# Optimization experiments

Measured on AMD Instinct MI355X. Metric: run time of the kernel, lower is better.

Reference implementation:

```python
import jax, jax.numpy as jnp
import numpy as np

D_MODEL = 1024
H = 16
T = 1024
B = 8

def setup_inputs() -> dict:
    key = jax.random.key(0)
    k0, k1, k2, k3, k4 = jax.random.split(key, 5)
    return {
        "x": jax.random.normal(k0, (B, T, D_MODEL), dtype=jnp.float32),
        "Wq": jax.random.normal(k1, (D_MODEL, D_MODEL), dtype=jnp.float32),
        "Wk": jax.random.normal(k2, (D_MODEL, D_MODEL), dtype=jnp.float32),
        "Wv": jax.random.normal(k3, (D_MODEL, D_MODEL), dtype=jnp.float32),
        "Wp": jax.random.normal(k4, (D_MODEL, D_MODEL), dtype=jnp.float32),
    }

def reference(x, Wq, Wk, Wv, Wp):
    b, t, d = x.shape
    dh = d // H
    # projections
    q = (x @ Wq).reshape(b, t, H, dh)
    k = (x @ Wk).reshape(b, t, H, dh)
    v = (x @ Wv).reshape(b, t, H, dh)
    # [b, h, t, t] attention scores, scaled by sqrt(d_head)
    scores = jnp.einsum("bqhd,bkhd->bhqk", q, k) / jnp.sqrt(jnp.float32(dh))
    attn = jax.nn.softmax(scores, axis=-1)
    # [b, h, t, dh] -> [b, t, d]
    out = jnp.einsum("bhqk,bkhd->bqhd", attn, v).reshape(b, t, d)
    return out @ Wp
```

## Files before the change

### kernel.cpp

```cpp
#include <hip/hip_runtime.h>
#include <math.h>


typedef unsigned short u16;
typedef unsigned int u32;
typedef __bf16  bf16x8 __attribute__((ext_vector_type(8)));
typedef unsigned short u16x8 __attribute__((ext_vector_type(8)));
typedef unsigned short u16x4 __attribute__((ext_vector_type(4)));
typedef short s16x4 __attribute__((ext_vector_type(4)));
typedef unsigned int u32x2 __attribute__((ext_vector_type(2)));
typedef float f32x4 __attribute__((ext_vector_type(4)));

#define MFMA16(a,b,c) __builtin_amdgcn_mfma_f32_16x16x32_bf16((a),(b),(c),0,0,0)
#define MFMA16K16(a,b,c) __builtin_amdgcn_mfma_f32_16x16x16bf16_1k((a),(b),(c),0,0,0)

static __device__ __forceinline__ u16 f2b(float f){
  unsigned u = __builtin_bit_cast(unsigned, f);
  u += 0x7fffu + ((u >> 16) & 1u);
  return (u16)(u >> 16);
}
static __device__ __forceinline__ float b2f(u16 h){
  unsigned u = ((unsigned)h) << 16;
  return __builtin_bit_cast(float, u);
}
static __device__ __forceinline__ bf16x8 ldsfrag(const u16* p){
  return __builtin_bit_cast(bf16x8, *(const u16x8*)p);
}
static __device__ __forceinline__ u32 packhi(float fa, float fb){
  return __builtin_amdgcn_perm(__builtin_bit_cast(u32, fa),
                               __builtin_bit_cast(u32, fb), 0x07060302u);
}
static __device__ __forceinline__ void gld16(const void* g, void* l){
  __builtin_amdgcn_global_load_lds(
      (const __attribute__((address_space(1))) void*)g,
      (__attribute__((address_space(3))) void*)l, 16, 0, 0);
}


__global__ __launch_bounds__(256) void split_x_kernel(
    const float* __restrict__ x, u16* __restrict__ xh, u16* __restrict__ xl, int n)
{
  int i = (blockIdx.x * 256 + threadIdx.x) * 8;
  if (i >= n) return;
  float4 v0 = *(const float4*)(x + i);
  float4 v1 = *(const float4*)(x + i + 4);
  float vv[8] = {v0.x, v0.y, v0.z, v0.w, v1.x, v1.y, v1.z, v1.w};
  u16x8 hv, lv;
#pragma unroll
  for (int j = 0; j < 8; j++){
    u16 hb = f2b(vv[j]);
    hv[j] = hb;
    lv[j] = f2b(vv[j] - b2f(hb));
  }
  *(u16x8*)(xh + i) = hv;
  *(u16x8*)(xl + i) = lv;
}

__global__ __launch_bounds__(256) void transpose_split_kernel(
    const float* __restrict__ W, u16* __restrict__ Th, u16* __restrict__ Tl,
    int KD, int ND)
{
  __shared__ float t[32][33];
  int n0 = blockIdx.x * 32, k0 = blockIdx.y * 32;
  int tx = threadIdx.x, ty = threadIdx.y;
#pragma unroll
  for (int i = 0; i < 4; i++){
    int k = k0 + ty + i * 8;
    t[ty + i * 8][tx] = W[(size_t)k * ND + n0 + tx];
  }
  __syncthreads();
#pragma unroll
  for (int i = 0; i < 4; i++){
    int n = n0 + ty + i * 8;
    float v = t[tx][ty + i * 8];
    u16 h = f2b(v);
    Th[(size_t)n * KD + k0 + tx] = h;
    if (Tl) Tl[(size_t)n * KD + k0 + tx] = f2b(v - b2f(h));
  }
}

__global__ __launch_bounds__(256) void vfrag_kernel(
    const u16* __restrict__ V, u16* __restrict__ Vf)
{
  int d = threadIdx.x;
  int tt = (blockIdx.x * 4 + threadIdx.y) * 4;
  int bh = blockIdx.y;
  int b = bh >> 4, h = bh & 15;
  u16x4 vals;
#pragma unroll
  for (int j = 0; j < 4; j++)
    vals[j] = V[(size_t)(b * 1024 + tt + j) * 1024 + h * 64 + d];
  int ktile = tt >> 7, fkt = (tt >> 4) & 7, q = (tt >> 2) & 3;
  int nd = d >> 4, l15 = d & 15;
  size_t idx = ((((size_t)(bh * 8 + ktile) * 8 + fkt) * 4 + nd) * 64 + q * 16 + l15) * 4;
  *(u16x4*)(Vf + idx) = vals;
}

template<int OUTBF16>
__global__ __launch_bounds__(256) void gemm_bt_kernel(
    const u16* __restrict__ A, const u16* __restrict__ Bt, void* __restrict__ Cv,
    int M, int N, int K)
{
  __shared__ __attribute__((aligned(16))) u16 lA[4096], lB[4096];
  const int tid = threadIdx.x, lane = tid & 63, wave = tid >> 6;
  const int quad = lane >> 4, l15 = lane & 15;
  const int row0 = blockIdx.x * 128, col0 = blockIdx.y * 128;
  const int wm = wave >> 1, wn = wave & 1;
  const int sr = lane >> 2, sc = (lane & 3) * 8;
  f32x4 acc[4][4];
#pragma unroll
  for (int mt = 0; mt < 4; mt++)
#pragma unroll
    for (int nt = 0; nt < 4; nt++) acc[mt][nt] = (f32x4)0.0f;

  for (int k0 = 0; k0 < K; k0 += 32){
#pragma unroll
    for (int i = 0; i < 2; i++){
      int c = wave * 2 + i;
      gld16(A  + (size_t)(row0 + c * 16 + sr) * K + k0 + sc, &lA[c * 512]);
      gld16(Bt + (size_t)(col0 + c * 16 + sr) * K + k0 + sc, &lB[c * 512]);
    }
    __syncthreads();
    bf16x8 a[4], b[4];
#pragma unroll
    for (int t = 0; t < 4; t++){
      a[t] = ldsfrag(&lA[(wm * 64 + t * 16 + l15) * 32 + quad * 8]);
      b[t] = ldsfrag(&lB[(wn * 64 + t * 16 + l15) * 32 + quad * 8]);
    }
#pragma unroll
    for (int mt = 0; mt < 4; mt++)
#pragma unroll
      for (int nt = 0; nt < 4; nt++)
        acc[mt][nt] = MFMA16(a[mt], b[nt], acc[mt][nt]);
    __syncthreads();
  }
#pragma unroll
  for (int mt = 0; mt < 4; mt++)
#pragma unroll
    for (int nt = 0; nt < 4; nt++)
#pragma unroll
      for (int r = 0; r < 4; r++){
        int row = row0 + wm * 64 + mt * 16 + quad * 4 + r;
        int col = col0 + wn * 64 + nt * 16 + l15;
        if (OUTBF16) ((u16*)Cv)[(size_t)row * N + col] = f2b(acc[mt][nt][r]);
        else         ((float*)Cv)[(size_t)row * N + col] = acc[mt][nt][r];
      }
}

__global__ __launch_bounds__(256) void gemm_qk_kernel(
    const u16* __restrict__ Ah, const u16* __restrict__ Al,
    const u16* __restrict__ Bh, const u16* __restrict__ Bl,
    u16* __restrict__ Qhf, u16* __restrict__ Qlf,
    u16* __restrict__ Khf, u16* __restrict__ Klf, int M, int N, int K)
{
  __shared__ __attribute__((aligned(16))) u16 lAh[4096], lAl[4096], lBh[4096], lBl[4096];
  const int tid = threadIdx.x, lane = tid & 63, wave = tid >> 6;
  const int quad = lane >> 4, l15 = lane & 15;
  const int row0 = blockIdx.x * 128, col0 = blockIdx.y * 128;
  const int wm = wave >> 1, wn = wave & 1;
  const int sr = lane >> 2, sc = (lane & 3) * 8;
  f32x4 acc[4][4];
#pragma unroll
  for (int mt = 0; mt < 4; mt++)
#pragma unroll
    for (int nt = 0; nt < 4; nt++) acc[mt][nt] = (f32x4)0.0f;

  for (int k0 = 0; k0 < K; k0 += 32){
#pragma unroll
    for (int i = 0; i < 2; i++){
      int c = wave * 2 + i;
      size_t ao = (size_t)(row0 + c * 16 + sr) * K + k0 + sc;
      size_t bo = (size_t)(col0 + c * 16 + sr) * K + k0 + sc;
      gld16(Ah + ao, &lAh[c * 512]);
      gld16(Al + ao, &lAl[c * 512]);
      gld16(Bh + bo, &lBh[c * 512]);
      gld16(Bl + bo, &lBl[c * 512]);
    }
    __syncthreads();
    bf16x8 ah[4], al[4], bh[4], bl[4];
#pragma unroll
    for (int t = 0; t < 4; t++){
      int aoff = (wm * 64 + t * 16 + l15) * 32 + quad * 8;
      int boff = (wn * 64 + t * 16 + l15) * 32 + quad * 8;
      ah[t] = ldsfrag(&lAh[aoff]);  al[t] = ldsfrag(&lAl[aoff]);
      bh[t] = ldsfrag(&lBh[boff]);  bl[t] = ldsfrag(&lBl[boff]);
    }
#pragma unroll
    for (int mt = 0; mt < 4; mt++)
#pragma unroll
      for (int nt = 0; nt < 4; nt++){
        acc[mt][nt] = MFMA16(al[mt], bh[nt], acc[mt][nt]);
        acc[mt][nt] = MFMA16(ah[mt], bl[nt], acc[mt][nt]);
        acc[mt][nt] = MFMA16(ah[mt], bh[nt], acc[mt][nt]);
      }
    __syncthreads();
  }
  const bool isQ = (col0 < 1024);
#pragma unroll
  for (int mt = 0; mt < 4; mt++)
#pragma unroll
    for (int nt = 0; nt < 4; nt++)
#pragma unroll
      for (int r = 0; r < 4; r++){
        int row = row0 + wm * 64 + mt * 16 + quad * 4 + r;
        int col = col0 + wn * 64 + nt * 16 + l15;
        int bb = row >> 10, tt = row & 1023;
        int hh = (col >> 6) & 15, d = col & 63;
        int bhI = bb * 16 + hh;
        int kc = d >> 5, qF = (d >> 3) & 3, j = d & 7;
        float v = acc[mt][nt][r];
        u16 hi = f2b(v);
        u16 lo = f2b(v - b2f(hi));
        if (isQ){
          int qtile = tt >> 7, rr = tt & 127;
          int wv = rr >> 5, mtF = (rr >> 4) & 1, l15F = tt & 15;
          size_t idx = ((((size_t)(bhI * 8 + qtile) * 4 + wv) * 2 + mtF) * 2 + kc) * 512
                       + (qF * 16 + l15F) * 8 + j;
          Qhf[idx] = hi; Qlf[idx] = lo;
        } else {
          int ktile = tt >> 7, fkt = (tt >> 4) & 7, l15F = tt & 15;
          size_t idx = (((size_t)(bhI * 8 + ktile) * 8 + fkt) * 2 + kc) * 512
                       + (qF * 16 + l15F) * 8 + j;
          Khf[idx] = hi; Klf[idx] = lo;
        }
      }
}

__global__ __launch_bounds__(256, 3) void attn_kernel(
    const u16* __restrict__ Qhf, const u16* __restrict__ Qlf,
    const u16* __restrict__ Khf, const u16* __restrict__ Klf,
    const u16* __restrict__ Vf, u16* __restrict__ O)
{
  __shared__ __attribute__((aligned(16))) u16 lKh[8192], lKl[8192], lV[8192];
  const int tid = threadIdx.x, lane = tid & 63, wave = tid >> 6;
  const int quad = lane >> 4, l15 = lane & 15;
  const int qt = blockIdx.x >> 7, bh = blockIdx.x & 127;
  const int b = bh >> 4, h = bh & 15;
  const int q0 = qt * 128;
  const float BETA = 0.18033688011112042f;

  bf16x8 qh[2][2], ql[2][2];
  {
    size_t qbase = (size_t)(bh * 8 + qt) * 8192 + wave * 2048 + lane * 8;
#pragma unroll
    for (int i = 0; i < 4; i++){
      gld16(Qhf + qbase + i * 512, &lKh[wave * 2048 + i * 512]);
      gld16(Qlf + qbase + i * 512, &lKl[wave * 2048 + i * 512]);
    }
    __syncthreads();
#pragma unroll
    for (int mt = 0; mt < 2; mt++)
#pragma unroll
      for (int kc = 0; kc < 2; kc++){
        int off = wave * 2048 + (mt * 2 + kc) * 512 + lane * 8;
        qh[mt][kc] = ldsfrag(&lKh[off]);
        ql[mt][kc] = ldsfrag(&lKl[off]);
      }
    __syncthreads();
  }

  float m_i[2] = {-3.0e38f, -3.0e38f}, l_i[2] = {0.0f, 0.0f};
  f32x4 o_acc[2][4];
#pragma unroll
  for (int mt = 0; mt < 2; mt++)
#pragma unroll
    for (int nd = 0; nd < 4; nd++) o_acc[mt][nd] = (f32x4)0.0f;

  for (int kt = 0; kt < 8; kt++){
    size_t kbase = (size_t)(bh * 8 + kt) * 8192 + wave * 2048 + lane * 8;
#pragma unroll
    for (int i = 0; i < 4; i++){
      gld16(Khf + kbase + i * 512, &lKh[wave * 2048 + i * 512]);
      gld16(Klf + kbase + i * 512, &lKl[wave * 2048 + i * 512]);
      gld16(Vf  + kbase + i * 512, &lV [wave * 2048 + i * 512]);
    }
    __syncthreads();

    f32x4 s[2][8];
#pragma unroll
    for (int qt2 = 0; qt2 < 2; qt2++)
#pragma unroll
      for (int fkt = 0; fkt < 8; fkt++) s[qt2][fkt] = (f32x4)0.0f;
#pragma unroll
    for (int fkt = 0; fkt < 8; fkt++){
      int aoff = fkt * 1024 + lane * 8;
      bf16x8 kh0 = ldsfrag(&lKh[aoff]);
      bf16x8 kh1 = ldsfrag(&lKh[aoff + 512]);
      bf16x8 kl0 = ldsfrag(&lKl[aoff]);
      bf16x8 kl1 = ldsfrag(&lKl[aoff + 512]);
#pragma unroll
      for (int qt2 = 0; qt2 < 2; qt2++){
        s[qt2][fkt] = MFMA16(kl0, qh[qt2][0], s[qt2][fkt]);
        s[qt2][fkt] = MFMA16(kl1, qh[qt2][1], s[qt2][fkt]);
        s[qt2][fkt] = MFMA16(kh0, ql[qt2][0], s[qt2][fkt]);
        s[qt2][fkt] = MFMA16(kh1, ql[qt2][1], s[qt2][fkt]);
        s[qt2][fkt] = MFMA16(kh0, qh[qt2][0], s[qt2][fkt]);
        s[qt2][fkt] = MFMA16(kh1, qh[qt2][1], s[qt2][fkt]);
      }
    }

    float alpha[2];
#pragma unroll
    for (int qt2 = 0; qt2 < 2; qt2++){
      float mx = s[qt2][0][0];
#pragma unroll
      for (int fkt = 0; fkt < 8; fkt++)
#pragma unroll
        for (int r = 0; r < 4; r++) mx = fmaxf(mx, s[qt2][fkt][r]);
      mx = fmaxf(mx, __shfl_xor(mx, 16));
      mx = fmaxf(mx, __shfl_xor(mx, 32));
      float mn = fmaxf(m_i[qt2], mx);
      alpha[qt2] = __builtin_amdgcn_exp2f((m_i[qt2] - mn) * BETA);
      m_i[qt2] = mn;
      float mb = mn * BETA;
      float rs = 0.0f;
#pragma unroll
      for (int fkt = 0; fkt < 8; fkt++)
#pragma unroll
        for (int r = 0; r < 4; r++){
          float p = __builtin_amdgcn_exp2f(s[qt2][fkt][r] * BETA - mb);
          s[qt2][fkt][r] = p;
          rs += p;
        }
      rs += __shfl_xor(rs, 16);
      rs += __shfl_xor(rs, 32);
      l_i[qt2] = l_i[qt2] * alpha[qt2] + rs;
    }

#pragma unroll
    for (int mt = 0; mt < 2; mt++)
#pragma unroll
      for (int r = 0; r < 4; r++){
        float ar = __shfl(alpha[mt], quad * 4 + r);
#pragma unroll
        for (int nd = 0; nd < 4; nd++) o_acc[mt][nd][r] *= ar;
      }

#pragma unroll
    for (int fkt = 0; fkt < 8; fkt++){
      s16x4 vb[4];
#pragma unroll
      for (int nd = 0; nd < 4; nd++)
        vb[nd] = __builtin_bit_cast(s16x4,
                   *(const u16x4*)&lV[(fkt * 4 + nd) * 256 + lane * 4]);
#pragma unroll
      for (int qt2 = 0; qt2 < 2; qt2++){
        u32x2 pd;
        pd[0] = packhi(s[qt2][fkt][1], s[qt2][fkt][0]);
        pd[1] = packhi(s[qt2][fkt][3], s[qt2][fkt][2]);
        s16x4 pa = __builtin_bit_cast(s16x4, pd);
#pragma unroll
        for (int nd = 0; nd < 4; nd++)
          o_acc[qt2][nd] = MFMA16K16(pa, vb[nd], o_acc[qt2][nd]);
      }
    }
    __syncthreads();
  }

#pragma unroll
  for (int mt = 0; mt < 2; mt++)
#pragma unroll
    for (int r = 0; r < 4; r++){
      float lr = __shfl(l_i[mt], quad * 4 + r);
      float inv = 1.0f / lr;
      int t = q0 + wave * 32 + mt * 16 + quad * 4 + r;
      size_t rowoff = (size_t)(b * 1024 + t) * 1024 + h * 64;
#pragma unroll
      for (int nd = 0; nd < 4; nd++)
        O[rowoff + nd * 16 + l15] = f2b(o_acc[mt][nd][r] * inv);
    }
}

extern "C" void kernel_launch(void* const* d_in, const int* in_sizes, int n_in,
                              void* d_out, int out_size, void* d_ws, size_t ws_size,
                              hipStream_t stream)
{
  const float* x  = (const float*)d_in[0];
  const float* Wq = (const float*)d_in[1];
  const float* Wk = (const float*)d_in[2];
  const float* Wv = (const float*)d_in[3];
  const float* Wp = (const float*)d_in[4];
  float* out = (float*)d_out;
  char* ws = (char*)d_ws;
  const size_t MB = 1024 * 1024;
  u16* xh   = (u16*)(ws + 0);
  u16* xl   = (u16*)(ws + 16 * MB);
  u16* wqkh = (u16*)(ws + 32 * MB);
  u16* wqkl = (u16*)(ws + 36 * MB);
  u16* wvt  = (u16*)(ws + 40 * MB);
  u16* wpt  = (u16*)(ws + 42 * MB);
  u16* Qhf  = (u16*)(ws + 44 * MB);
  u16* Qlf  = (u16*)(ws + 60 * MB);
  u16* Khf  = (u16*)(ws + 76 * MB);
  u16* Klf  = (u16*)(ws + 92 * MB);
  u16* Vf   = (u16*)(ws + 108 * MB);
  u16* vbuf = xl;
  u16* obuf = xh;
  (void)in_sizes; (void)n_in; (void)out_size; (void)ws_size;

  dim3 tb(32, 8);
  split_x_kernel<<<4096, 256, 0, stream>>>(x, xh, xl, 8 * 1024 * 1024);
  transpose_split_kernel<<<dim3(32, 32), tb, 0, stream>>>(Wq, wqkh, wqkl, 1024, 1024);
  transpose_split_kernel<<<dim3(32, 32), tb, 0, stream>>>(Wk, wqkh + 1024 * 1024, wqkl + 1024 * 1024, 1024, 1024);
  transpose_split_kernel<<<dim3(32, 32), tb, 0, stream>>>(Wv, wvt, (u16*)nullptr, 1024, 1024);
  transpose_split_kernel<<<dim3(32, 32), tb, 0, stream>>>(Wp, wpt, (u16*)nullptr, 1024, 1024);
  gemm_qk_kernel<<<dim3(64, 16), 256, 0, stream>>>(xh, xl, wqkh, wqkl,
                                                   Qhf, Qlf, Khf, Klf, 8192, 2048, 1024);
  gemm_bt_kernel<1><<<dim3(64, 8), 256, 0, stream>>>(xh, wvt, (void*)vbuf, 8192, 1024, 1024);
  vfrag_kernel<<<dim3(64, 128), dim3(64, 4), 0, stream>>>(vbuf, Vf);
  attn_kernel<<<1024, 256, 0, stream>>>(Qhf, Qlf, Khf, Klf, Vf, obuf);
  gemm_bt_kernel<0><<<dim3(64, 8), 256, 0, stream>>>(obuf, wpt, (void*)out, 8192, 1024, 1024);
}
```

Before: 397.0 us.

## Fuse V fragment layout into V GEMM epilogue and double attention block size

The V projection GEMM now writes its bf16 output straight into the fragment layout the attention kernel consumes, so the separate vfrag reshuffle kernel and its intermediate buffer go away. The attention kernel moves to 512-thread blocks covering 256 query rows, so each K/V tile loaded into LDS serves twice as many queries and global K/V traffic is halved. Q hi/lo loads now go through one shared staging buffer in two passes. The cost is larger blocks with fewer of them (512), which can hurt occupancy or the tail on the GPU.

```diff
diff --git a/kernel.cpp b/kernel.cpp
--- a/kernel.cpp
+++ b/kernel.cpp
@@ -79,24 +79,7 @@
   }
 }
 
-__global__ __launch_bounds__(256) void vfrag_kernel(
-    const u16* __restrict__ V, u16* __restrict__ Vf)
-{
-  int d = threadIdx.x;
-  int tt = (blockIdx.x * 4 + threadIdx.y) * 4;
-  int bh = blockIdx.y;
-  int b = bh >> 4, h = bh & 15;
-  u16x4 vals;
-#pragma unroll
-  for (int j = 0; j < 4; j++)
-    vals[j] = V[(size_t)(b * 1024 + tt + j) * 1024 + h * 64 + d];
-  int ktile = tt >> 7, fkt = (tt >> 4) & 7, q = (tt >> 2) & 3;
-  int nd = d >> 4, l15 = d & 15;
-  size_t idx = ((((size_t)(bh * 8 + ktile) * 8 + fkt) * 4 + nd) * 64 + q * 16 + l15) * 4;
-  *(u16x4*)(Vf + idx) = vals;
-}
-
-template<int OUTBF16>
+template<int OUTMODE>
 __global__ __launch_bounds__(256) void gemm_bt_kernel(
     const u16* __restrict__ A, const u16* __restrict__ Bt, void* __restrict__ Cv,
     int M, int N, int K)
@@ -134,17 +117,37 @@
         acc[mt][nt] = MFMA16(a[mt], b[nt], acc[mt][nt]);
     __syncthreads();
   }
-#pragma unroll
-  for (int mt = 0; mt < 4; mt++)
-#pragma unroll
-    for (int nt = 0; nt < 4; nt++)
-#pragma unroll
-      for (int r = 0; r < 4; r++){
-        int row = row0 + wm * 64 + mt * 16 + quad * 4 + r;
+  if (OUTMODE == 2){
+#pragma unroll
+    for (int mt = 0; mt < 4; mt++)
+#pragma unroll
+      for (int nt = 0; nt < 4; nt++){
+        int row = row0 + wm * 64 + mt * 16 + quad * 4;
         int col = col0 + wn * 64 + nt * 16 + l15;
-        if (OUTBF16) ((u16*)Cv)[(size_t)row * N + col] = f2b(acc[mt][nt][r]);
-        else         ((float*)Cv)[(size_t)row * N + col] = acc[mt][nt][r];
-      }
+        int bb = row >> 10, tt = row & 1023;
+        int hh = (col >> 6) & 15, d = col & 63;
+        int bhI = bb * 16 + hh;
+        int ktile = tt >> 7, fkt = (tt >> 4) & 7, qF = (tt >> 2) & 3;
+        int nd = d >> 4, l15F = d & 15;
+        size_t idx = ((((size_t)(bhI * 8 + ktile) * 8 + fkt) * 4 + nd) * 64
+                      + qF * 16 + l15F) * 4;
+        u16x4 vals;
+#pragma unroll
+        for (int r = 0; r < 4; r++) vals[r] = f2b(acc[mt][nt][r]);
+        *(u16x4*)(((u16*)Cv) + idx) = vals;
+      }
+  } else {
+#pragma unroll
+    for (int mt = 0; mt < 4; mt++)
+#pragma unroll
+      for (int nt = 0; nt < 4; nt++)
+#pragma unroll
+        for (int r = 0; r < 4; r++){
+          int row = row0 + wm * 64 + mt * 16 + quad * 4 + r;
+          int col = col0 + wn * 64 + nt * 16 + l15;
+          ((float*)Cv)[(size_t)row * N + col] = acc[mt][nt][r];
+        }
+  }
 }
 
 __global__ __launch_bounds__(256) void gemm_qk_kernel(
@@ -226,36 +229,45 @@
       }
 }
 
-__global__ __launch_bounds__(256, 3) void attn_kernel(
+__global__ __launch_bounds__(512, 4) void attn_kernel(
     const u16* __restrict__ Qhf, const u16* __restrict__ Qlf,
     const u16* __restrict__ Khf, const u16* __restrict__ Klf,
     const u16* __restrict__ Vf, u16* __restrict__ O)
 {
-  __shared__ __attribute__((aligned(16))) u16 lKh[8192], lKl[8192], lV[8192];
+  __shared__ __attribute__((aligned(16))) u16 lds[24576];
+  u16* lKh = lds;
+  u16* lKl = lds + 8192;
+  u16* lV  = lds + 16384;
   const int tid = threadIdx.x, lane = tid & 63, wave = tid >> 6;
   const int quad = lane >> 4, l15 = lane & 15;
   const int qt = blockIdx.x >> 7, bh = blockIdx.x & 127;
   const int b = bh >> 4, h = bh & 15;
-  const int q0 = qt * 128;
+  const int q0 = qt * 256;
   const float BETA = 0.18033688011112042f;
 
   bf16x8 qh[2][2], ql[2][2];
   {
-    size_t qbase = (size_t)(bh * 8 + qt) * 8192 + wave * 2048 + lane * 8;
-#pragma unroll
-    for (int i = 0; i < 4; i++){
-      gld16(Qhf + qbase + i * 512, &lKh[wave * 2048 + i * 512]);
-      gld16(Qlf + qbase + i * 512, &lKl[wave * 2048 + i * 512]);
-    }
+    int qtileL = qt * 2 + (wave >> 2), wv = wave & 3;
+    size_t qbase = ((size_t)(bh * 8 + qtileL) * 4 + wv) * 2048 + lane * 8;
+#pragma unroll
+    for (int i = 0; i < 4; i++)
+      gld16(Qhf + qbase + i * 512, &lds[wave * 2048 + i * 512]);
     __syncthreads();
 #pragma unroll
     for (int mt = 0; mt < 2; mt++)
 #pragma unroll
-      for (int kc = 0; kc < 2; kc++){
-        int off = wave * 2048 + (mt * 2 + kc) * 512 + lane * 8;
-        qh[mt][kc] = ldsfrag(&lKh[off]);
-        ql[mt][kc] = ldsfrag(&lKl[off]);
-      }
+      for (int kc = 0; kc < 2; kc++)
+        qh[mt][kc] = ldsfrag(&lds[wave * 2048 + (mt * 2 + kc) * 512 + lane * 8]);
+    __syncthreads();
+#pragma unroll
+    for (int i = 0; i < 4; i++)
+      gld16(Qlf + qbase + i * 512, &lds[wave * 2048 + i * 512]);
+    __syncthreads();
+#pragma unroll
+    for (int mt = 0; mt < 2; mt++)
+#pragma unroll
+      for (int kc = 0; kc < 2; kc++)
+        ql[mt][kc] = ldsfrag(&lds[wave * 2048 + (mt * 2 + kc) * 512 + lane * 8]);
     __syncthreads();
   }
 
@@ -267,12 +279,13 @@
     for (int nd = 0; nd < 4; nd++) o_acc[mt][nd] = (f32x4)0.0f;
 
   for (int kt = 0; kt < 8; kt++){
-    size_t kbase = (size_t)(bh * 8 + kt) * 8192 + wave * 2048 + lane * 8;
-#pragma unroll
-    for (int i = 0; i < 4; i++){
-      gld16(Khf + kbase + i * 512, &lKh[wave * 2048 + i * 512]);
-      gld16(Klf + kbase + i * 512, &lKl[wave * 2048 + i * 512]);
-      gld16(Vf  + kbase + i * 512, &lV [wave * 2048 + i * 512]);
+    size_t kpan = (size_t)(bh * 8 + kt) * 8192;
+#pragma unroll
+    for (int i = 0; i < 2; i++){
+      int c = wave * 2 + i;
+      gld16(Khf + kpan + c * 512 + lane * 8, &lKh[c * 512]);
+      gld16(Klf + kpan + c * 512 + lane * 8, &lKl[c * 512]);
+      gld16(Vf  + kpan + c * 512 + lane * 8, &lV [c * 512]);
     }
     __syncthreads();
 
@@ -394,7 +407,6 @@
   u16* Khf  = (u16*)(ws + 76 * MB);
   u16* Klf  = (u16*)(ws + 92 * MB);
   u16* Vf   = (u16*)(ws + 108 * MB);
-  u16* vbuf = xl;
   u16* obuf = xh;
   (void)in_sizes; (void)n_in; (void)out_size; (void)ws_size;
 
@@ -406,8 +418,7 @@
   transpose_split_kernel<<<dim3(32, 32), tb, 0, stream>>>(Wp, wpt, (u16*)nullptr, 1024, 1024);
   gemm_qk_kernel<<<dim3(64, 16), 256, 0, stream>>>(xh, xl, wqkh, wqkl,
                                                    Qhf, Qlf, Khf, Klf, 8192, 2048, 1024);
-  gemm_bt_kernel<1><<<dim3(64, 8), 256, 0, stream>>>(xh, wvt, (void*)vbuf, 8192, 1024, 1024);
-  vfrag_kernel<<<dim3(64, 128), dim3(64, 4), 0, stream>>>(vbuf, Vf);
-  attn_kernel<<<1024, 256, 0, stream>>>(Qhf, Qlf, Khf, Klf, Vf, obuf);
+  gemm_bt_kernel<2><<<dim3(64, 8), 256, 0, stream>>>(xh, wvt, (void*)Vf, 8192, 1024, 1024);
+  attn_kernel<<<512, 512, 0, stream>>>(Qhf, Qlf, Khf, Klf, Vf, obuf);
   gemm_bt_kernel<0><<<dim3(64, 8), 256, 0, stream>>>(obuf, wpt, (void*)out, 8192, 1024, 1024);
 }
```

After: 443.3 us. 11.7% more time.

## Fuse V fragment reordering into V GEMM epilogue and split attention tile into halves

Applied to the files above, without the earlier changes.

The V projection GEMM now writes its bf16 output directly in the MFMA-fragment layout the attention kernel consumes, which removes the separate vfrag kernel and its extra read and write pass over V. Separately, the attention inner loop processes each 128-key tile in two halves of 64 keys with a non-unrolled loop and its own online softmax update. The split halves the live score registers, aiming at lower register pressure or higher occupancy, at the cost of an extra rescale step and more max/sum reductions per tile.

```diff
diff --git a/kernel.cpp b/kernel.cpp
--- a/kernel.cpp
+++ b/kernel.cpp
@@ -79,24 +79,7 @@
   }
 }
 
-__global__ __launch_bounds__(256) void vfrag_kernel(
-    const u16* __restrict__ V, u16* __restrict__ Vf)
-{
-  int d = threadIdx.x;
-  int tt = (blockIdx.x * 4 + threadIdx.y) * 4;
-  int bh = blockIdx.y;
-  int b = bh >> 4, h = bh & 15;
-  u16x4 vals;
-#pragma unroll
-  for (int j = 0; j < 4; j++)
-    vals[j] = V[(size_t)(b * 1024 + tt + j) * 1024 + h * 64 + d];
-  int ktile = tt >> 7, fkt = (tt >> 4) & 7, q = (tt >> 2) & 3;
-  int nd = d >> 4, l15 = d & 15;
-  size_t idx = ((((size_t)(bh * 8 + ktile) * 8 + fkt) * 4 + nd) * 64 + q * 16 + l15) * 4;
-  *(u16x4*)(Vf + idx) = vals;
-}
-
-template<int OUTBF16>
+template<int OUTMODE>
 __global__ __launch_bounds__(256) void gemm_bt_kernel(
     const u16* __restrict__ A, const u16* __restrict__ Bt, void* __restrict__ Cv,
     int M, int N, int K)
@@ -134,17 +117,37 @@
         acc[mt][nt] = MFMA16(a[mt], b[nt], acc[mt][nt]);
     __syncthreads();
   }
-#pragma unroll
-  for (int mt = 0; mt < 4; mt++)
-#pragma unroll
-    for (int nt = 0; nt < 4; nt++)
-#pragma unroll
-      for (int r = 0; r < 4; r++){
-        int row = row0 + wm * 64 + mt * 16 + quad * 4 + r;
+  if (OUTMODE == 2){
+#pragma unroll
+    for (int mt = 0; mt < 4; mt++)
+#pragma unroll
+      for (int nt = 0; nt < 4; nt++){
+        int row = row0 + wm * 64 + mt * 16 + quad * 4;
         int col = col0 + wn * 64 + nt * 16 + l15;
-        if (OUTBF16) ((u16*)Cv)[(size_t)row * N + col] = f2b(acc[mt][nt][r]);
-        else         ((float*)Cv)[(size_t)row * N + col] = acc[mt][nt][r];
-      }
+        int bb = row >> 10, tt = row & 1023;
+        int hh = (col >> 6) & 15, d = col & 63;
+        int bhI = bb * 16 + hh;
+        int ktile = tt >> 7, fkt = (tt >> 4) & 7, qF = (tt >> 2) & 3;
+        int nd = d >> 4, l15F = d & 15;
+        size_t idx = ((((size_t)(bhI * 8 + ktile) * 8 + fkt) * 4 + nd) * 64
+                      + qF * 16 + l15F) * 4;
+        u16x4 vals;
+#pragma unroll
+        for (int r = 0; r < 4; r++) vals[r] = f2b(acc[mt][nt][r]);
+        *(u16x4*)(((u16*)Cv) + idx) = vals;
+      }
+  } else {
+#pragma unroll
+    for (int mt = 0; mt < 4; mt++)
+#pragma unroll
+      for (int nt = 0; nt < 4; nt++)
+#pragma unroll
+        for (int r = 0; r < 4; r++){
+          int row = row0 + wm * 64 + mt * 16 + quad * 4 + r;
+          int col = col0 + wn * 64 + nt * 16 + l15;
+          ((float*)Cv)[(size_t)row * N + col] = acc[mt][nt][r];
+        }
+  }
 }
 
 __global__ __launch_bounds__(256) void gemm_qk_kernel(
@@ -276,82 +279,86 @@
     }
     __syncthreads();
 
-    f32x4 s[2][8];
-#pragma unroll
-    for (int qt2 = 0; qt2 < 2; qt2++)
-#pragma unroll
-      for (int fkt = 0; fkt < 8; fkt++) s[qt2][fkt] = (f32x4)0.0f;
-#pragma unroll
-    for (int fkt = 0; fkt < 8; fkt++){
-      int aoff = fkt * 1024 + lane * 8;
-      bf16x8 kh0 = ldsfrag(&lKh[aoff]);
-      bf16x8 kh1 = ldsfrag(&lKh[aoff + 512]);
-      bf16x8 kl0 = ldsfrag(&lKl[aoff]);
-      bf16x8 kl1 = ldsfrag(&lKl[aoff + 512]);
+#pragma unroll 1
+    for (int half = 0; half < 2; half++){
+      f32x4 s[2][4];
+#pragma unroll
+      for (int qt2 = 0; qt2 < 2; qt2++)
+#pragma unroll
+        for (int f4 = 0; f4 < 4; f4++) s[qt2][f4] = (f32x4)0.0f;
+#pragma unroll
+      for (int f4 = 0; f4 < 4; f4++){
+        int aoff = (half * 4 + f4) * 1024 + lane * 8;
+        bf16x8 kh0 = ldsfrag(&lKh[aoff]);
+        bf16x8 kh1 = ldsfrag(&lKh[aoff + 512]);
+        bf16x8 kl0 = ldsfrag(&lKl[aoff]);
+        bf16x8 kl1 = ldsfrag(&lKl[aoff + 512]);
+#pragma unroll
+        for (int qt2 = 0; qt2 < 2; qt2++){
+          s[qt2][f4] = MFMA16(kl0, qh[qt2][0], s[qt2][f4]);
+          s[qt2][f4] = MFMA16(kl1, qh[qt2][1], s[qt2][f4]);
+          s[qt2][f4] = MFMA16(kh0, ql[qt2][0], s[qt2][f4]);
+          s[qt2][f4] = MFMA16(kh1, ql[qt2][1], s[qt2][f4]);
+          s[qt2][f4] = MFMA16(kh0, qh[qt2][0], s[qt2][f4]);
+          s[qt2][f4] = MFMA16(kh1, qh[qt2][1], s[qt2][f4]);
+        }
+      }
+
+      float alpha[2];
 #pragma unroll
       for (int qt2 = 0; qt2 < 2; qt2++){
-        s[qt2][fkt] = MFMA16(kl0, qh[qt2][0], s[qt2][fkt]);
-        s[qt2][fkt] = MFMA16(kl1, qh[qt2][1], s[qt2][fkt]);
-        s[qt2][fkt] = MFMA16(kh0, ql[qt2][0], s[qt2][fkt]);
-        s[qt2][fkt] = MFMA16(kh1, ql[qt2][1], s[qt2][fkt]);
-        s[qt2][fkt] = MFMA16(kh0, qh[qt2][0], s[qt2][fkt]);
-        s[qt2][fkt] = MFMA16(kh1, qh[qt2][1], s[qt2][fkt]);
-      }
-    }
-
-    float alpha[2];
-#pragma unroll
-    for (int qt2 = 0; qt2 < 2; qt2++){
-      float mx = s[qt2][0][0];
-#pragma unroll
-      for (int fkt = 0; fkt < 8; fkt++)
-#pragma unroll
-        for (int r = 0; r < 4; r++) mx = fmaxf(mx, s[qt2][fkt][r]);
-      mx = fmaxf(mx, __shfl_xor(mx, 16));
-      mx = fmaxf(mx, __shfl_xor(mx, 32));
-      float mn = fmaxf(m_i[qt2], mx);
-      alpha[qt2] = __builtin_amdgcn_exp2f((m_i[qt2] - mn) * BETA);
-      m_i[qt2] = mn;
-      float mb = mn * BETA;
-      float rs = 0.0f;
-#pragma unroll
-      for (int fkt = 0; fkt < 8; fkt++)
+        float mx = s[qt2][0][0];
+#pragma unroll
+        for (int f4 = 0; f4 < 4; f4++)
+#pragma unroll
+          for (int r = 0; r < 4; r++) mx = fmaxf(mx, s[qt2][f4][r]);
+        mx = fmaxf(mx, __shfl_xor(mx, 16));
+        mx = fmaxf(mx, __shfl_xor(mx, 32));
+        float mn = fmaxf(m_i[qt2], mx);
+        alpha[qt2] = __builtin_amdgcn_exp2f((m_i[qt2] - mn) * BETA);
+        m_i[qt2] = mn;
+        float mb = mn * BETA;
+        float rs = 0.0f;
+#pragma unroll
+        for (int f4 = 0; f4 < 4; f4++)
+#pragma unroll
+          for (int r = 0; r < 4; r++){
+            float p = __builtin_amdgcn_exp2f(s[qt2][f4][r] * BETA - mb);
+            s[qt2][f4][r] = p;
+            rs += p;
+          }
+        rs += __shfl_xor(rs, 16);
+        rs += __shfl_xor(rs, 32);
+        l_i[qt2] = l_i[qt2] * alpha[qt2] + rs;
+      }
+
+#pragma unroll
+      for (int mt = 0; mt < 2; mt++)
 #pragma unroll
         for (int r = 0; r < 4; r++){
-          float p = __builtin_amdgcn_exp2f(s[qt2][fkt][r] * BETA - mb);
-          s[qt2][fkt][r] = p;
-          rs += p;
+          float ar = __shfl(alpha[mt], quad * 4 + r);
+#pragma unroll
+          for (int nd = 0; nd < 4; nd++) o_acc[mt][nd][r] *= ar;
         }
-      rs += __shfl_xor(rs, 16);
-      rs += __shfl_xor(rs, 32);
-      l_i[qt2] = l_i[qt2] * alpha[qt2] + rs;
-    }
-
-#pragma unroll
-    for (int mt = 0; mt < 2; mt++)
-#pragma unroll
-      for (int r = 0; r < 4; r++){
-        float ar = __shfl(alpha[mt], quad * 4 + r);
-#pragma unroll
-        for (int nd = 0; nd < 4; nd++) o_acc[mt][nd][r] *= ar;
-      }
-
-#pragma unroll
-    for (int fkt = 0; fkt < 8; fkt++){
-      s16x4 vb[4];
-#pragma unroll
-      for (int nd = 0; nd < 4; nd++)
-        vb[nd] = __builtin_bit_cast(s16x4,
-                   *(const u16x4*)&lV[(fkt * 4 + nd) * 256 + lane * 4]);
-#pragma unroll
-      for (int qt2 = 0; qt2 < 2; qt2++){
-        u32x2 pd;
-        pd[0] = packhi(s[qt2][fkt][1], s[qt2][fkt][0]);
-        pd[1] = packhi(s[qt2][fkt][3], s[qt2][fkt][2]);
-        s16x4 pa = __builtin_bit_cast(s16x4, pd);
+
+#pragma unroll
+      for (int f4 = 0; f4 < 4; f4++){
+        int fkt = half * 4 + f4;
+        s16x4 vb[4];
 #pragma unroll
         for (int nd = 0; nd < 4; nd++)
-          o_acc[qt2][nd] = MFMA16K16(pa, vb[nd], o_acc[qt2][nd]);
+          vb[nd] = __builtin_bit_cast(s16x4,
+                     *(const u16x4*)&lV[(fkt * 4 + nd) * 256 + lane * 4]);
+#pragma unroll
+        for (int qt2 = 0; qt2 < 2; qt2++){
+          u32x2 pd;
+          pd[0] = packhi(s[qt2][f4][1], s[qt2][f4][0]);
+          pd[1] = packhi(s[qt2][f4][3], s[qt2][f4][2]);
+          s16x4 pa = __builtin_bit_cast(s16x4, pd);
+#pragma unroll
+          for (int nd = 0; nd < 4; nd++)
+            o_acc[qt2][nd] = MFMA16K16(pa, vb[nd], o_acc[qt2][nd]);
+        }
       }
     }
     __syncthreads();
@@ -394,7 +401,6 @@
   u16* Khf  = (u16*)(ws + 76 * MB);
   u16* Klf  = (u16*)(ws + 92 * MB);
   u16* Vf   = (u16*)(ws + 108 * MB);
-  u16* vbuf = xl;
   u16* obuf = xh;
   (void)in_sizes; (void)n_in; (void)out_size; (void)ws_size;
 
@@ -406,8 +412,7 @@
   transpose_split_kernel<<<dim3(32, 32), tb, 0, stream>>>(Wp, wpt, (u16*)nullptr, 1024, 1024);
   gemm_qk_kernel<<<dim3(64, 16), 256, 0, stream>>>(xh, xl, wqkh, wqkl,
                                                    Qhf, Qlf, Khf, Klf, 8192, 2048, 1024);
-  gemm_bt_kernel<1><<<dim3(64, 8), 256, 0, stream>>>(xh, wvt, (void*)vbuf, 8192, 1024, 1024);
-  vfrag_kernel<<<dim3(64, 128), dim3(64, 4), 0, stream>>>(vbuf, Vf);
+  gemm_bt_kernel<2><<<dim3(64, 8), 256, 0, stream>>>(xh, wvt, (void*)Vf, 8192, 1024, 1024);
   attn_kernel<<<1024, 256, 0, stream>>>(Qhf, Qlf, Khf, Klf, Vf, obuf);
   gemm_bt_kernel<0><<<dim3(64, 8), 256, 0, stream>>>(obuf, wpt, (void*)out, 8192, 1024, 1024);
 }
```

After: 359.0 us. 9.6% less time.
